# Kernel optimization log

Hardware: AMD Instinct MI355X
Metric: run time of the kernel (lower is better)

## Reference

```python
import jax, jax.numpy as jnp
import numpy as np

B, D, E = 2048, 2048, 64
EPS = 1e-8

def setup_inputs() -> dict:
    key = jax.random.key(0)
    kx, kw, kb = jax.random.split(key, 3)
    # scale weights like torch Linear default init (uniform ~ 1/sqrt(D)); use scaled normal
    return {
        "x": jax.random.normal(kx, (B, D), dtype=jnp.float32),
        "W": jax.random.normal(kw, (E * E, D), dtype=jnp.float32) / np.sqrt(D),
        "b": jax.random.normal(kb, (E * E,), dtype=jnp.float32) / np.sqrt(D),
        "reg": jnp.asarray(0.01, dtype=jnp.float32),
    }

def reference(x, W, b, reg):
    # Linear projection: [B, D] @ [D, E*E] + b -> [B, E*E]
    m = jnp.einsum("bd,ed->be", x, W) + b
    m = m.reshape(-1, E, E)
    # Symmetrize and regularize diagonal
    m = (m + jnp.swapaxes(m, 1, 2)) * 0.5
    m = m + reg * jnp.eye(E, dtype=m.dtype)
    # Batched symmetric eigendecomposition (ascending eigenvalues)
    eigenvals = jnp.linalg.eigvalsh(m)  # [B, E]
    # Descending order, log-clamped
    eigenvals = jnp.flip(eigenvals, axis=1)
    return jnp.log(jnp.clip(eigenvals, EPS, None))
```

## Files before the change

### kernel.cpp

```cpp
#include <hip/hip_runtime.h>

typedef __bf16 bf16x8 __attribute__((ext_vector_type(8)));
typedef float f32x4 __attribute__((ext_vector_type(4)));

union U8 { uint4 u; bf16x8 b; };

__device__ inline float bf16f(unsigned short h) {
    return __uint_as_float(((unsigned)h) << 16);
}

__device__ inline unsigned short f32_to_bf16_rn(float f) {
    unsigned u = __float_as_uint(f);
    unsigned rounding = 0x7FFFu + ((u >> 16) & 1u);
    u += rounding;
    return (unsigned short)(u >> 16);
}

__device__ inline double wsum(double v) {
    #pragma unroll
    for (int m = 32; m; m >>= 1) v += __shfl_xor(v, m, 64);
    return v;
}
__device__ inline double wmin(double v) {
    #pragma unroll
    for (int m = 32; m; m >>= 1) v = fmin(v, __shfl_xor(v, m, 64));
    return v;
}
__device__ inline double wmax(double v) {
    #pragma unroll
    for (int m = 32; m; m >>= 1) v = fmax(v, __shfl_xor(v, m, 64));
    return v;
}

#define AS1C(p) ((const __attribute__((address_space(1))) void*)(p))
#define AS3(p)  ((__attribute__((address_space(3))) void*)(p))

__global__ __launch_bounds__(256) void split2(
    const float* __restrict__ X, const float* __restrict__ W,
    const float* __restrict__ b, const float* __restrict__ regp,
    unsigned short* __restrict__ Xh, unsigned short* __restrict__ Xm, unsigned short* __restrict__ Xl,
    unsigned short* __restrict__ Sh, unsigned short* __restrict__ Sm, unsigned short* __restrict__ Sl,
    float* __restrict__ bsym)
{
    size_t i4 = (size_t)blockIdx.x * 256 + threadIdx.x;

    if (i4 < 1048576) {
        float4 v = ((const float4*)X)[i4];
        ushort4 h, m, l; float r1;
        h.x = f32_to_bf16_rn(v.x); r1 = v.x - bf16f(h.x);
        m.x = f32_to_bf16_rn(r1);  l.x = f32_to_bf16_rn(r1 - bf16f(m.x));
        h.y = f32_to_bf16_rn(v.y); r1 = v.y - bf16f(h.y);
        m.y = f32_to_bf16_rn(r1);  l.y = f32_to_bf16_rn(r1 - bf16f(m.y));
        h.z = f32_to_bf16_rn(v.z); r1 = v.z - bf16f(h.z);
        m.z = f32_to_bf16_rn(r1);  l.z = f32_to_bf16_rn(r1 - bf16f(m.z));
        h.w = f32_to_bf16_rn(v.w); r1 = v.w - bf16f(h.w);
        m.w = f32_to_bf16_rn(r1);  l.w = f32_to_bf16_rn(r1 - bf16f(m.w));
        ((ushort4*)Xh)[i4] = h;
        ((ushort4*)Xm)[i4] = m;
        ((ushort4*)Xl)[i4] = l;
        return;
    }

    size_t q = i4 - 1048576;
    int p  = (int)(q >> 9);
    int d4 = (int)(q & 511);

    if (p >= 2080) {
        ushort4 z; z.x = 0; z.y = 0; z.z = 0; z.w = 0;
        ((ushort4*)Sh)[q] = z; ((ushort4*)Sm)[q] = z; ((ushort4*)Sl)[q] = z;
        if (d4 == 0) bsym[p] = 0.0f;
        return;
    }

    double sd = sqrt(16641.0 - 8.0 * (double)p);
    int i = (int)((129.0 - sd) * 0.5);
    if (i < 0) i = 0;
    if (i > 63) i = 63;
    while (i < 63 && ((i + 1) * (128 - i)) / 2 <= p) ++i;
    while (i > 0 && (i * (129 - i)) / 2 > p) --i;
    int j = i + (p - (i * (129 - i)) / 2);
    int e1 = i * 64 + j;
    int e2 = j * 64 + i;

    float4 v1 = ((const float4*)W)[(size_t)e1 * 512 + d4];
    float4 v2 = ((const float4*)W)[(size_t)e2 * 512 + d4];
    float4 v;
    v.x = 0.5f * (v1.x + v2.x);
    v.y = 0.5f * (v1.y + v2.y);
    v.z = 0.5f * (v1.z + v2.z);
    v.w = 0.5f * (v1.w + v2.w);

    ushort4 h, m, l; float r1;
    h.x = f32_to_bf16_rn(v.x); r1 = v.x - bf16f(h.x);
    m.x = f32_to_bf16_rn(r1);  l.x = f32_to_bf16_rn(r1 - bf16f(m.x));
    h.y = f32_to_bf16_rn(v.y); r1 = v.y - bf16f(h.y);
    m.y = f32_to_bf16_rn(r1);  l.y = f32_to_bf16_rn(r1 - bf16f(m.y));
    h.z = f32_to_bf16_rn(v.z); r1 = v.z - bf16f(h.z);
    m.z = f32_to_bf16_rn(r1);  l.z = f32_to_bf16_rn(r1 - bf16f(m.z));
    h.w = f32_to_bf16_rn(v.w); r1 = v.w - bf16f(h.w);
    m.w = f32_to_bf16_rn(r1);  l.w = f32_to_bf16_rn(r1 - bf16f(m.w));
    ((ushort4*)Sh)[q] = h;
    ((ushort4*)Sm)[q] = m;
    ((ushort4*)Sl)[q] = l;

    if (d4 == 0)
        bsym[p] = 0.5f * (b[e1] + b[e2]) + ((i == j) ? regp[0] : 0.0f);
}

__global__ __launch_bounds__(256) void gemm_packed(
    const unsigned short* __restrict__ Xh, const unsigned short* __restrict__ Xm,
    const unsigned short* __restrict__ Xl,
    const unsigned short* __restrict__ Sh, const unsigned short* __restrict__ Sm,
    const unsigned short* __restrict__ Sl,
    const float* __restrict__ bsym, float* __restrict__ Mp)
{
    const int K = 2048, NP = 2112;
    __shared__ unsigned short S[18432];

    int tid  = threadIdx.x;
    int id   = blockIdx.x;
    int c    = id & 7;
    int sid  = id >> 3;
    int wg   = c * 66 + sid;
    int bx   = wg % 33;
    int by   = wg / 33;
    int m0   = by * 128;
    int n0   = bx * 64;

    int wave = tid >> 6;
    int lane = tid & 63;
    int l16  = lane & 15;
    int quad = lane >> 4;
    int wm   = wave * 32;

    const unsigned short* gpA[3];
    const unsigned short* gpB[3];
    gpA[0] = Xh + (size_t)m0 * K;
    gpA[1] = Xm + (size_t)m0 * K;
    gpA[2] = Xl + (size_t)m0 * K;
    gpB[0] = Sh + (size_t)n0 * K;
    gpB[1] = Sm + (size_t)n0 * K;
    gpB[2] = Sl + (size_t)n0 * K;

    int rA = lane >> 2;
    int cA = (lane & 3) << 3;

    f32x4 acc[2][4];
    #pragma unroll
    for (int mi = 0; mi < 2; ++mi)
        #pragma unroll
        for (int ni = 0; ni < 4; ++ni)
            acc[mi][ni] = f32x4{0.f, 0.f, 0.f, 0.f};

    for (int k0 = 0; k0 < K; k0 += 32) {
        __syncthreads();
        #pragma unroll
        for (int p = 0; p < 3; ++p) {
            #pragma unroll
            for (int q = 0; q < 2; ++q) {
                const unsigned short* g = gpA[p] + (size_t)(32 * wave + 16 * q + rA) * K + k0 + cA;
                char* l = (char*)S + p * 8192 + wave * 2048 + q * 1024;
                __builtin_amdgcn_global_load_lds(AS1C(g), AS3(l), 16, 0, 0);
            }
            {
                const unsigned short* g = gpB[p] + (size_t)(16 * wave + rA) * K + k0 + cA;
                char* l = (char*)S + 24576 + p * 4096 + wave * 1024;
                __builtin_amdgcn_global_load_lds(AS1C(g), AS3(l), 16, 0, 0);
            }
        }
        __syncthreads();

        U8 ah[2], am[2], al[2], bh[4], bm[4], bl[4];
        #pragma unroll
        for (int mi = 0; mi < 2; ++mi) {
            int ro = (wm + mi * 16 + l16) * 32 + quad * 8;
            ah[mi].u = *(const uint4*)&S[ro];
            am[mi].u = *(const uint4*)&S[4096 + ro];
            al[mi].u = *(const uint4*)&S[8192 + ro];
        }
        #pragma unroll
        for (int ni = 0; ni < 4; ++ni) {
            int ro = (ni * 16 + l16) * 32 + quad * 8;
            bh[ni].u = *(const uint4*)&S[12288 + ro];
            bm[ni].u = *(const uint4*)&S[14336 + ro];
            bl[ni].u = *(const uint4*)&S[16384 + ro];
        }

        #pragma unroll
        for (int mi = 0; mi < 2; ++mi)
            #pragma unroll
            for (int ni = 0; ni < 4; ++ni) {
                acc[mi][ni] = __builtin_amdgcn_mfma_f32_16x16x32_bf16(
                    al[mi].b, bh[ni].b, acc[mi][ni], 0, 0, 0);
                acc[mi][ni] = __builtin_amdgcn_mfma_f32_16x16x32_bf16(
                    ah[mi].b, bl[ni].b, acc[mi][ni], 0, 0, 0);
                acc[mi][ni] = __builtin_amdgcn_mfma_f32_16x16x32_bf16(
                    am[mi].b, bm[ni].b, acc[mi][ni], 0, 0, 0);
                acc[mi][ni] = __builtin_amdgcn_mfma_f32_16x16x32_bf16(
                    am[mi].b, bh[ni].b, acc[mi][ni], 0, 0, 0);
                acc[mi][ni] = __builtin_amdgcn_mfma_f32_16x16x32_bf16(
                    ah[mi].b, bm[ni].b, acc[mi][ni], 0, 0, 0);
                acc[mi][ni] = __builtin_amdgcn_mfma_f32_16x16x32_bf16(
                    ah[mi].b, bh[ni].b, acc[mi][ni], 0, 0, 0);
            }
    }

    #pragma unroll
    for (int ni = 0; ni < 4; ++ni) {
        int col = n0 + ni * 16 + l16;
        float bv = bsym[col];
        #pragma unroll
        for (int mi = 0; mi < 2; ++mi) {
            int row = m0 + wm + mi * 16 + quad * 4;
            #pragma unroll
            for (int r = 0; r < 4; ++r)
                Mp[(size_t)(row + r) * NP + col] = acc[mi][ni][r] + bv;
        }
    }
}

__global__ __launch_bounds__(128, 4) void tridiag_packed2(
    const float* __restrict__ Mp, double* __restrict__ trid)
{
    __shared__ __align__(16) float Ls[2112];
    __shared__ __align__(16) double rowb[64];
    __shared__ __align__(16) double ubuf[64];
    __shared__ __align__(16) double wbuf[64];
    __shared__ __align__(16) double pps[128];
    __shared__ double dbuf[64];
    __shared__ double ebuf[64];

    int g   = blockIdx.x;
    int tid = threadIdx.x;
    int h   = tid >> 6;
    int t   = tid & 63;
    int base = 32 * h;

    const float4* Pg = (const float4*)(Mp + (size_t)g * 2112);
    float4* L4 = (float4*)Ls;
    #pragma unroll
    for (int s = 0; s < 4; ++s)
        L4[s * 128 + tid] = Pg[s * 128 + tid];
    if (tid < 16) L4[512 + tid] = Pg[512 + tid];
    __syncthreads();

    double A[32];
    #pragma unroll
    for (int jj = 0; jj < 32; ++jj) {
        int cj = base + jj;
        int lo = (t < cj) ? t : cj;
        int hi = t + cj - lo;
        int idx = ((lo * (129 - lo)) >> 1) + (hi - lo);
        A[jj] = (double)Ls[idx];
    }

    #pragma unroll 1
    for (int k = 0; k < 32; ++k) {
        if (t == k) {
            #pragma unroll
            for (int jj = 0; jj < 16; ++jj)
                *(double2*)&rowb[base + 2 * jj] = double2{A[2 * jj], A[2 * jj + 1]};
        }
        __syncthreads();

        double x  = rowb[t];
        double x1 = rowb[k + 1];
        double xm = (t > k) ? x : 0.0;
        double sigma = wsum(xm * xm);

        double alpha = 0.0, u = 0.0, w = 0.0, rK = 0.0;
        bool run = (sigma > 1e-300);
        if (run) {
            double sq = sqrt(sigma);
            alpha = (x1 >= 0.0) ? -sq : sq;
            rK = 1.0 / (sigma - x1 * alpha);
            u = (t == k + 1) ? (x - alpha) : xm;
        }
        if (h == 0) ubuf[t] = u;
        if (tid == 0) { dbuf[k] = rowb[k]; ebuf[k] = alpha; }
        __syncthreads();

        double ph = 0.0;
        if (run) {
            double p0 = 0.0, p1 = 0.0;
            #pragma unroll
            for (int jj = 0; jj < 16; ++jj) {
                double2 uv = *(const double2*)&ubuf[base + 2 * jj];
                p0 += A[2 * jj]     * uv.x;
                p1 += A[2 * jj + 1] * uv.y;
            }
            ph = p0 + p1;
        }
        pps[h * 64 + t] = ph;
        __syncthreads();

        if (run) {
            double p = (t > k) ? (pps[t] + pps[64 + t]) * rK : 0.0;
            double cc = wsum(u * p) * (0.5 * rK);
            w = p - cc * u;
        }
        if (h == 0) wbuf[t] = w;
        __syncthreads();

        if (run) {
            #pragma unroll
            for (int jj = 0; jj < 16; ++jj) {
                double2 uv = *(const double2*)&ubuf[base + 2 * jj];
                double2 wv = *(const double2*)&wbuf[base + 2 * jj];
                A[2 * jj]     -= u * wv.x + w * uv.x;
                A[2 * jj + 1] -= u * wv.y + w * uv.y;
            }
        }
    }

    #pragma unroll 1
    for (int k = 32; k < 62; ++k) {
        if (h == 1 && t == k) {
            #pragma unroll
            for (int jj = 0; jj < 16; ++jj)
                *(double2*)&rowb[32 + 2 * jj] = double2{A[2 * jj], A[2 * jj + 1]};
        }
        __syncthreads();

        double u = 0.0, w = 0.0, rK = 0.0;
        bool run = false;
        if (h == 1) {
            double x  = rowb[t];
            double x1 = rowb[k + 1];
            double xm = (t > k) ? x : 0.0;
            double sigma = wsum(xm * xm);
            double alpha = 0.0;
            run = (sigma > 1e-300);
            if (run) {
                double sq = sqrt(sigma);
                alpha = (x1 >= 0.0) ? -sq : sq;
                rK = 1.0 / (sigma - x1 * alpha);
                u = (t == k + 1) ? (x - alpha) : xm;
            }
            ubuf[t] = u;
            if (t == 0) { dbuf[k] = rowb[k]; ebuf[k] = alpha; }
        }
        __syncthreads();

        if (h == 1) {
            if (run) {
                double p0 = 0.0, p1 = 0.0;
                #pragma unroll
                for (int jj = 0; jj < 16; ++jj) {
                    double2 uv = *(const double2*)&ubuf[32 + 2 * jj];
                    p0 += A[2 * jj]     * uv.x;
                    p1 += A[2 * jj + 1] * uv.y;
                }
                double p = (t > k) ? (p0 + p1) * rK : 0.0;
                double cc = wsum(u * p) * (0.5 * rK);
                w = p - cc * u;
            }
            wbuf[t] = w;
        }
        __syncthreads();

        if (h == 1 && run) {
            #pragma unroll
            for (int jj = 0; jj < 16; ++jj) {
                double2 uv = *(const double2*)&ubuf[32 + 2 * jj];
                double2 wv = *(const double2*)&wbuf[32 + 2 * jj];
                A[2 * jj]     -= u * wv.x + w * uv.x;
                A[2 * jj + 1] -= u * wv.y + w * uv.y;
            }
        }
    }

    if (h == 1 && t == 62) dbuf[62] = A[30];
    if (h == 1 && t == 63) { dbuf[63] = A[31];
                             ebuf[62] = A[30]; }
    if (tid == 0) ebuf[63] = 0.0;
    __syncthreads();

    if (h == 0) {
        double* tg = trid + (size_t)g * 128;
        tg[t]      = dbuf[t];
        tg[64 + t] = ebuf[t];
    }
}

__global__ __launch_bounds__(256) void gemm_bt(const float* __restrict__ Xf,
                                               const float* __restrict__ Wf,
                                               const float* __restrict__ biasf,
                                               float* __restrict__ M)
{
    const int K = 2048, N = 4096;
    __shared__ unsigned short AsH[128][32];
    __shared__ unsigned short AsM[128][32];
    __shared__ unsigned short AsL[128][32];
    __shared__ unsigned short BsH[128][32];
    __shared__ unsigned short BsM[128][32];
    __shared__ unsigned short BsL[128][32];

    int tid  = threadIdx.x;
    int m0   = blockIdx.y * 128;
    int n0   = blockIdx.x * 128;
    int wid  = tid >> 6;
    int lane = tid & 63;
    int wm   = (wid >> 1) * 64;
    int wn   = (wid & 1) * 64;
    int l16  = lane & 15;
    int quad = lane >> 4;

    f32x4 acc[4][4];
    #pragma unroll
    for (int mi = 0; mi < 4; ++mi)
        #pragma unroll
        for (int ni = 0; ni < 4; ++ni)
            acc[mi][ni] = f32x4{0.f, 0.f, 0.f, 0.f};

    for (int k0 = 0; k0 < K; k0 += 32) {
        #pragma unroll
        for (int s = 0; s < 4; ++s) {
            int c  = tid + s * 256;
            int r  = c >> 3;
            int kc = (c & 7) << 2;
            {
                float4 v = *(const float4*)&Xf[(size_t)(m0 + r) * K + k0 + kc];
                ushort4 h, mm_, l; float r1;
                h.x = f32_to_bf16_rn(v.x); r1 = v.x - bf16f(h.x);
                mm_.x = f32_to_bf16_rn(r1); l.x = f32_to_bf16_rn(r1 - bf16f(mm_.x));
                h.y = f32_to_bf16_rn(v.y); r1 = v.y - bf16f(h.y);
                mm_.y = f32_to_bf16_rn(r1); l.y = f32_to_bf16_rn(r1 - bf16f(mm_.y));
                h.z = f32_to_bf16_rn(v.z); r1 = v.z - bf16f(h.z);
                mm_.z = f32_to_bf16_rn(r1); l.z = f32_to_bf16_rn(r1 - bf16f(mm_.z));
                h.w = f32_to_bf16_rn(v.w); r1 = v.w - bf16f(h.w);
                mm_.w = f32_to_bf16_rn(r1); l.w = f32_to_bf16_rn(r1 - bf16f(mm_.w));
                *(ushort4*)&AsH[r][kc] = h; *(ushort4*)&AsM[r][kc] = mm_; *(ushort4*)&AsL[r][kc] = l;
            }
            {
                float4 v = *(const float4*)&Wf[(size_t)(n0 + r) * K + k0 + kc];
                ushort4 h, mm_, l; float r1;
                h.x = f32_to_bf16_rn(v.x); r1 = v.x - bf16f(h.x);
                mm_.x = f32_to_bf16_rn(r1); l.x = f32_to_bf16_rn(r1 - bf16f(mm_.x));
                h.y = f32_to_bf16_rn(v.y); r1 = v.y - bf16f(h.y);
                mm_.y = f32_to_bf16_rn(r1); l.y = f32_to_bf16_rn(r1 - bf16f(mm_.y));
                h.z = f32_to_bf16_rn(v.z); r1 = v.z - bf16f(h.z);
                mm_.z = f32_to_bf16_rn(r1); l.z = f32_to_bf16_rn(r1 - bf16f(mm_.z));
                h.w = f32_to_bf16_rn(v.w); r1 = v.w - bf16f(h.w);
                mm_.w = f32_to_bf16_rn(r1); l.w = f32_to_bf16_rn(r1 - bf16f(mm_.w));
                *(ushort4*)&BsH[r][kc] = h; *(ushort4*)&BsM[r][kc] = mm_; *(ushort4*)&BsL[r][kc] = l;
            }
        }
        __syncthreads();

        U8 ah[4], am[4], al[4], bh[4], bm[4], bl[4];
        #pragma unroll
        for (int mi = 0; mi < 4; ++mi) {
            ah[mi].u = *(const uint4*)&AsH[wm + mi * 16 + l16][quad * 8];
            am[mi].u = *(const uint4*)&AsM[wm + mi * 16 + l16][quad * 8];
            al[mi].u = *(const uint4*)&AsL[wm + mi * 16 + l16][quad * 8];
        }
        #pragma unroll
        for (int ni = 0; ni < 4; ++ni) {
            bh[ni].u = *(const uint4*)&BsH[wn + ni * 16 + l16][quad * 8];
            bm[ni].u = *(const uint4*)&BsM[wn + ni * 16 + l16][quad * 8];
            bl[ni].u = *(const uint4*)&BsL[wn + ni * 16 + l16][quad * 8];
        }

        #pragma unroll
        for (int mi = 0; mi < 4; ++mi)
            #pragma unroll
            for (int ni = 0; ni < 4; ++ni) {
                acc[mi][ni] = __builtin_amdgcn_mfma_f32_16x16x32_bf16(al[mi].b, bh[ni].b, acc[mi][ni], 0, 0, 0);
                acc[mi][ni] = __builtin_amdgcn_mfma_f32_16x16x32_bf16(ah[mi].b, bl[ni].b, acc[mi][ni], 0, 0, 0);
                acc[mi][ni] = __builtin_amdgcn_mfma_f32_16x16x32_bf16(am[mi].b, bm[ni].b, acc[mi][ni], 0, 0, 0);
                acc[mi][ni] = __builtin_amdgcn_mfma_f32_16x16x32_bf16(am[mi].b, bh[ni].b, acc[mi][ni], 0, 0, 0);
                acc[mi][ni] = __builtin_amdgcn_mfma_f32_16x16x32_bf16(ah[mi].b, bm[ni].b, acc[mi][ni], 0, 0, 0);
                acc[mi][ni] = __builtin_amdgcn_mfma_f32_16x16x32_bf16(ah[mi].b, bh[ni].b, acc[mi][ni], 0, 0, 0);
            }
        __syncthreads();
    }

    #pragma unroll
    for (int ni = 0; ni < 4; ++ni) {
        int col = n0 + wn + ni * 16 + l16;
        float bv = biasf[col];
        #pragma unroll
        for (int mi = 0; mi < 4; ++mi) {
            int row = m0 + wm + mi * 16 + quad * 4;
            #pragma unroll
            for (int r = 0; r < 4; ++r)
                M[(size_t)(row + r) * N + col] = acc[mi][ni][r] + bv;
        }
    }
}

__global__ __launch_bounds__(64, 2) void tridiag_full(const float* __restrict__ M,
                                                      const float* __restrict__ regf,
                                                      double* __restrict__ trid)
{
    __shared__ float Ms[64][65];
    __shared__ __align__(16) double rowb[64];
    __shared__ __align__(16) double ubuf[64];
    __shared__ __align__(16) double wbuf[64];
    __shared__ double dbuf[64];
    __shared__ double ebuf[64];

    int g = blockIdx.x;
    int t = threadIdx.x;
    const float* Mg = M + (size_t)g * 4096;

    for (int r = 0; r < 64; ++r)
        Ms[r][t] = Mg[r * 64 + t];
    __syncthreads();

    double regv = (double)regf[0];
    double A[64];
    #pragma unroll
    for (int j = 0; j < 64; ++j)
        A[j] = 0.5 * ((double)Ms[t][j] + (double)Ms[j][t]);
    #pragma unroll
    for (int j = 0; j < 64; ++j)
        A[j] += (j == t) ? regv : 0.0;

    #pragma unroll 1
    for (int k = 0; k < 62; ++k) {
        if (t == k) {
            #pragma unroll
            for (int j = 0; j < 32; ++j)
                *(double2*)&rowb[2 * j] = double2{A[2 * j], A[2 * j + 1]};
        }
        __syncthreads();

        double s0 = 0.0, s1 = 0.0;
        #pragma unroll
        for (int j = 0; j < 64; ++j) {
            double aj = (j > k) ? A[j] : 0.0;
            if (j & 1) s1 += aj * aj; else s0 += aj * aj;
        }
        double sigma = __shfl(s0 + s1, k, 64);
        double x  = rowb[t];
        double x1 = __shfl(x, k + 1, 64);

        double alpha = 0.0, u = 0.0, w = 0.0, Kh = 1.0;
        bool run = (sigma > 1e-300);
        if (run) {
            double sq = sqrt(sigma);
            alpha = (x1 >= 0.0) ? -sq : sq;
            Kh = sigma - x1 * alpha;
            u = (t == k + 1) ? (x - alpha) : ((t > k) ? x : 0.0);
        }
        ubuf[t] = u;
        if (t == 0) { dbuf[k] = rowb[k]; ebuf[k] = alpha; }
        __syncthreads();

        if (run) {
            double p0 = 0.0, p1 = 0.0;
            #pragma unroll
            for (int j = 0; j < 32; ++j) {
                double2 uv = *(const double2*)&ubuf[2 * j];
                p0 += A[2 * j]     * uv.x;
                p1 += A[2 * j + 1] * uv.y;
            }
            double p = (t > k) ? (p0 + p1) / Kh : 0.0;
            double cc = wsum(u * p) / (2.0 * Kh);
            w = p - cc * u;
        }
        wbuf[t] = w;
        __syncthreads();

        if (run) {
            #pragma unroll
            for (int j = 0; j < 32; ++j) {
                double2 uv = *(const double2*)&ubuf[2 * j];
                double2 wv = *(const double2*)&wbuf[2 * j];
                A[2 * j]     -= u * wv.x + w * uv.x;
                A[2 * j + 1] -= u * wv.y + w * uv.y;
            }
        }
        __syncthreads();
    }

    if (t == 62) dbuf[62] = A[62];
    if (t == 63) { dbuf[63] = A[63]; ebuf[62] = A[62]; }
    if (t == 0)  ebuf[63] = 0.0;
    __syncthreads();

    double* tg = trid + (size_t)g * 128;
    tg[t]      = dbuf[t];
    tg[64 + t] = ebuf[t];
}

__global__ __launch_bounds__(64) void bisect_kernel(const double* __restrict__ trid,
                                                    float* __restrict__ out)
{
    __shared__ double dd[64];
    __shared__ double e2[64];
    __shared__ double ea[64];

    int g = blockIdx.x;
    int t = threadIdx.x;
    const double* tg = trid + (size_t)g * 128;

    double dv = tg[t];
    double ev = tg[64 + t];
    dd[t] = dv;
    ea[t] = fabs(ev);
    e2[t] = ev * ev;
    __syncthreads();

    double el  = (t > 0) ? ea[t - 1] : 0.0;
    double er  = (t < 63) ? ea[t] : 0.0;
    double rad = el + er;
    double lo = wmin(dv - rad);
    double hi = wmax(dv + rad);
    double mid0 = 0.5 * (lo + hi);
    double half = (0.5 * (hi - lo) + 1e-12) * 1.0000001;
    double a = mid0 - half;
    double b = mid0 + half;

    for (int it = 0; it < 30; ++it) {
        double xm = 0.5 * (a + b);
        double pm = 1.0;
        double p  = dd[0] - xm;
        int cnt = (p < 0.0);
        #pragma unroll
        for (int i = 1; i < 64; ++i) {
            double pi = (dd[i] - xm) * p - e2[i - 1] * pm;
            cnt += ((pi < 0.0) != (p < 0.0));
            double ap = fabs(pi);
            double s = (ap > 1e150) ? 1e-150 : ((ap < 1e-150) ? 1e150 : 1.0);
            pm = p * s;
            p  = pi * s;
        }
        if (cnt > t) b = xm; else a = xm;
    }

    double lam = 0.5 * (a + b);
    double v = fmax(lam, 1e-8);
    out[(size_t)g * 64 + (63 - t)] = (float)log(v);
}

extern "C" void kernel_launch(void* const* d_in, const int* in_sizes, int n_in,
                              void* d_out, int out_size, void* d_ws, size_t ws_size,
                              hipStream_t stream)
{
    const float* X    = (const float*)d_in[0];
    const float* Wt   = (const float*)d_in[1];
    const float* bias = (const float*)d_in[2];
    const float* regp = (const float*)d_in[3];

    char* w = (char*)d_ws;
    float* out = (float*)d_out;

    const size_t NEED_FAST = 70525184ull;
    if (ws_size >= NEED_FAST) {
        float*  Mp   = (float*)w;
        double* trid = (double*)(w + 17301504);
        unsigned short* Xh = (unsigned short*)(w + 19398656);
        unsigned short* Xm = (unsigned short*)(w + 27787264);
        unsigned short* Xl = (unsigned short*)(w + 36175872);
        unsigned short* Sh = (unsigned short*)(w + 44564480);
        unsigned short* Sm = (unsigned short*)(w + 53215232);
        unsigned short* Sl = (unsigned short*)(w + 61865984);
        float* bsym = (float*)(w + 70516736);
        split2<<<dim3(8320), dim3(256), 0, stream>>>(X, Wt, bias, regp,
                                                     Xh, Xm, Xl, Sh, Sm, Sl, bsym);
        gemm_packed<<<dim3(528), dim3(256), 0, stream>>>(Xh, Xm, Xl, Sh, Sm, Sl, bsym, Mp);
        tridiag_packed2<<<dim3(2048), dim3(128), 0, stream>>>(Mp, trid);
        bisect_kernel<<<dim3(2048), dim3(64), 0, stream>>>(trid, out);
    } else {
        float*  M    = (float*)w;
        double* trid = (double*)(w + 33554432);
        gemm_bt<<<dim3(32, 16), dim3(256), 0, stream>>>(X, Wt, bias, M);
        tridiag_full<<<dim3(2048), dim3(64), 0, stream>>>(M, regp, trid);
        bisect_kernel<<<dim3(2048), dim3(64), 0, stream>>>(trid, out);
    }
}
```

Before: 609.4 us.

## Split GEMM along K into two partial outputs and streamline tridiagonalization reductions

After: 651.6 us. 6.9% more time.

```diff
diff --git a/kernel.cpp b/kernel.cpp
--- a/kernel.cpp
+++ b/kernel.cpp
@@ -30,6 +30,36 @@
     #pragma unroll
     for (int m = 32; m; m >>= 1) v = fmax(v, __shfl_xor(v, m, 64));
     return v;
+}
+
+__device__ inline double dpp_sum64(double v) {
+    union DU { double d; int i[2]; };
+    DU x, t; x.d = v;
+    t.i[0] = __builtin_amdgcn_update_dpp(0, x.i[0], 0xB1, 0xF, 0xF, true);
+    t.i[1] = __builtin_amdgcn_update_dpp(0, x.i[1], 0xB1, 0xF, 0xF, true);
+    x.d += t.d;
+    t.i[0] = __builtin_amdgcn_update_dpp(0, x.i[0], 0x4E, 0xF, 0xF, true);
+    t.i[1] = __builtin_amdgcn_update_dpp(0, x.i[1], 0x4E, 0xF, 0xF, true);
+    x.d += t.d;
+    t.i[0] = __builtin_amdgcn_update_dpp(0, x.i[0], 0x141, 0xF, 0xF, true);
+    t.i[1] = __builtin_amdgcn_update_dpp(0, x.i[1], 0x141, 0xF, 0xF, true);
+    x.d += t.d;
+    t.i[0] = __builtin_amdgcn_update_dpp(0, x.i[0], 0x140, 0xF, 0xF, true);
+    t.i[1] = __builtin_amdgcn_update_dpp(0, x.i[1], 0x140, 0xF, 0xF, true);
+    x.d += t.d;
+    t.i[0] = __builtin_amdgcn_update_dpp(0, x.i[0], 0x142, 0xF, 0xF, true);
+    t.i[1] = __builtin_amdgcn_update_dpp(0, x.i[1], 0x142, 0xF, 0xF, true);
+    x.d += t.d;
+    t.i[0] = __builtin_amdgcn_update_dpp(0, x.i[0], 0x143, 0xF, 0xF, true);
+    t.i[1] = __builtin_amdgcn_update_dpp(0, x.i[1], 0x143, 0xF, 0xF, true);
+    x.d += t.d;
+    int lo = __builtin_amdgcn_readlane(x.i[0], 63);
+    int hi = __builtin_amdgcn_readlane(x.i[1], 63);
+    return __hiloint2double(hi, lo);
+}
+
+__device__ inline float4 f4add(float4 a, float4 b) {
+    return float4{a.x + b.x, a.y + b.y, a.z + b.z, a.w + b.w};
 }
 
 #define AS1C(p) ((const __attribute__((address_space(1))) void*)(p))
@@ -121,11 +151,14 @@
     int id   = blockIdx.x;
     int c    = id & 7;
     int sid  = id >> 3;
-    int wg   = c * 66 + sid;
+    int kh   = (sid >= 66) ? 1 : 0;
+    int sidh = sid - kh * 66;
+    int wg   = c * 66 + sidh;
     int bx   = wg % 33;
     int by   = wg / 33;
     int m0   = by * 128;
     int n0   = bx * 64;
+    int kb   = kh * 1024;
 
     int wave = tid >> 6;
     int lane = tid & 63;
@@ -152,7 +185,7 @@
         for (int ni = 0; ni < 4; ++ni)
             acc[mi][ni] = f32x4{0.f, 0.f, 0.f, 0.f};
 
-    for (int k0 = 0; k0 < K; k0 += 32) {
+    for (int k0 = kb; k0 < kb + 1024; k0 += 32) {
         __syncthreads();
         #pragma unroll
         for (int p = 0; p < 3; ++p) {
@@ -205,28 +238,28 @@
             }
     }
 
+    float* Mout = Mp + (size_t)kh * 4325376;
     #pragma unroll
     for (int ni = 0; ni < 4; ++ni) {
         int col = n0 + ni * 16 + l16;
-        float bv = bsym[col];
+        float bv = kh ? 0.0f : bsym[col];
         #pragma unroll
         for (int mi = 0; mi < 2; ++mi) {
             int row = m0 + wm + mi * 16 + quad * 4;
             #pragma unroll
             for (int r = 0; r < 4; ++r)
-                Mp[(size_t)(row + r) * NP + col] = acc[mi][ni][r] + bv;
-        }
-    }
-}
-
-__global__ __launch_bounds__(128, 4) void tridiag_packed2(
+                Mout[(size_t)(row + r) * NP + col] = acc[mi][ni][r] + bv;
+        }
+    }
+}
+
+__global__ __launch_bounds__(128, 3) void tridiag_packed3(
     const float* __restrict__ Mp, double* __restrict__ trid)
 {
     __shared__ __align__(16) float Ls[2112];
     __shared__ __align__(16) double rowb[64];
-    __shared__ __align__(16) double ubuf[64];
     __shared__ __align__(16) double wbuf[64];
-    __shared__ __align__(16) double pps[128];
+    __shared__ __align__(16) double pps2[128];
     __shared__ double dbuf[64];
     __shared__ double ebuf[64];
 
@@ -236,12 +269,13 @@
     int t   = tid & 63;
     int base = 32 * h;
 
-    const float4* Pg = (const float4*)(Mp + (size_t)g * 2112);
+    const float4* Pg0 = (const float4*)(Mp + (size_t)g * 2112);
+    const float4* Pg1 = (const float4*)(Mp + 4325376 + (size_t)g * 2112);
     float4* L4 = (float4*)Ls;
     #pragma unroll
     for (int s = 0; s < 4; ++s)
-        L4[s * 128 + tid] = Pg[s * 128 + tid];
-    if (tid < 16) L4[512 + tid] = Pg[512 + tid];
+        L4[s * 128 + tid] = f4add(Pg0[s * 128 + tid], Pg1[s * 128 + tid]);
+    if (tid < 16) L4[512 + tid] = f4add(Pg0[512 + tid], Pg1[512 + tid]);
     __syncthreads();
 
     double A[32];
@@ -266,49 +300,50 @@
         double x  = rowb[t];
         double x1 = rowb[k + 1];
         double xm = (t > k) ? x : 0.0;
-        double sigma = wsum(xm * xm);
-
+        double sigma = dpp_sum64(xm * xm);
+
+        bool run = (sigma > 1e-300);
         double alpha = 0.0, u = 0.0, w = 0.0, rK = 0.0;
-        bool run = (sigma > 1e-300);
+        double uc[32];
+        double ph = 0.0;
         if (run) {
             double sq = sqrt(sigma);
             alpha = (x1 >= 0.0) ? -sq : sq;
             rK = 1.0 / (sigma - x1 * alpha);
             u = (t == k + 1) ? (x - alpha) : xm;
-        }
-        if (h == 0) ubuf[t] = u;
+            double p0 = 0.0, p1 = 0.0;
+            #pragma unroll
+            for (int jj = 0; jj < 16; ++jj) {
+                double2 rv = *(const double2*)&rowb[base + 2 * jj];
+                int j0 = base + 2 * jj, j1 = base + 2 * jj + 1;
+                double u0 = (j0 == k + 1) ? (rv.x - alpha) : ((j0 > k) ? rv.x : 0.0);
+                double u1 = (j1 == k + 1) ? (rv.y - alpha) : ((j1 > k) ? rv.y : 0.0);
+                uc[2 * jj]     = u0;
+                uc[2 * jj + 1] = u1;
+                p0 += A[2 * jj]     * u0;
+                p1 += A[2 * jj + 1] * u1;
+            }
+            ph = p0 + p1;
+        }
+        pps2[2 * t + h] = ph;
         if (tid == 0) { dbuf[k] = rowb[k]; ebuf[k] = alpha; }
         __syncthreads();
 
-        double ph = 0.0;
         if (run) {
-            double p0 = 0.0, p1 = 0.0;
+            double2 pp = *(const double2*)&pps2[2 * t];
+            double p = (t > k) ? (pp.x + pp.y) * rK : 0.0;
+            double cc = dpp_sum64(u * p) * (0.5 * rK);
+            w = p - cc * u;
+        }
+        if (h == 0) wbuf[t] = w;
+        __syncthreads();
+
+        if (run) {
             #pragma unroll
             for (int jj = 0; jj < 16; ++jj) {
-                double2 uv = *(const double2*)&ubuf[base + 2 * jj];
-                p0 += A[2 * jj]     * uv.x;
-                p1 += A[2 * jj + 1] * uv.y;
-            }
-            ph = p0 + p1;
-        }
-        pps[h * 64 + t] = ph;
-        __syncthreads();
-
-        if (run) {
-            double p = (t > k) ? (pps[t] + pps[64 + t]) * rK : 0.0;
-            double cc = wsum(u * p) * (0.5 * rK);
-            w = p - cc * u;
-        }
-        if (h == 0) wbuf[t] = w;
-        __syncthreads();
-
-        if (run) {
-            #pragma unroll
-            for (int jj = 0; jj < 16; ++jj) {
-                double2 uv = *(const double2*)&ubuf[base + 2 * jj];
                 double2 wv = *(const double2*)&wbuf[base + 2 * jj];
-                A[2 * jj]     -= u * wv.x + w * uv.x;
-                A[2 * jj + 1] -= u * wv.y + w * uv.y;
+                A[2 * jj]     -= u * wv.x + w * uc[2 * jj];
+                A[2 * jj + 1] -= u * wv.y + w * uc[2 * jj + 1];
             }
         }
     }
@@ -322,50 +357,48 @@
         }
         __syncthreads();
 
-        double u = 0.0, w = 0.0, rK = 0.0;
+        double u = 0.0, w = 0.0;
         bool run = false;
+        double uc[32];
         if (h == 1) {
             double x  = rowb[t];
             double x1 = rowb[k + 1];
             double xm = (t > k) ? x : 0.0;
-            double sigma = wsum(xm * xm);
+            double sigma = dpp_sum64(xm * xm);
             double alpha = 0.0;
             run = (sigma > 1e-300);
             if (run) {
                 double sq = sqrt(sigma);
                 alpha = (x1 >= 0.0) ? -sq : sq;
-                rK = 1.0 / (sigma - x1 * alpha);
+                double rK = 1.0 / (sigma - x1 * alpha);
                 u = (t == k + 1) ? (x - alpha) : xm;
-            }
-            ubuf[t] = u;
-            if (t == 0) { dbuf[k] = rowb[k]; ebuf[k] = alpha; }
-        }
-        __syncthreads();
-
-        if (h == 1) {
-            if (run) {
                 double p0 = 0.0, p1 = 0.0;
                 #pragma unroll
                 for (int jj = 0; jj < 16; ++jj) {
-                    double2 uv = *(const double2*)&ubuf[32 + 2 * jj];
-                    p0 += A[2 * jj]     * uv.x;
-                    p1 += A[2 * jj + 1] * uv.y;
+                    double2 rv = *(const double2*)&rowb[32 + 2 * jj];
+                    int j0 = 32 + 2 * jj, j1 = 33 + 2 * jj;
+                    double u0 = (j0 == k + 1) ? (rv.x - alpha) : ((j0 > k) ? rv.x : 0.0);
+                    double u1 = (j1 == k + 1) ? (rv.y - alpha) : ((j1 > k) ? rv.y : 0.0);
+                    uc[2 * jj]     = u0;
+                    uc[2 * jj + 1] = u1;
+                    p0 += A[2 * jj]     * u0;
+                    p1 += A[2 * jj + 1] * u1;
                 }
                 double p = (t > k) ? (p0 + p1) * rK : 0.0;
-                double cc = wsum(u * p) * (0.5 * rK);
+                double cc = dpp_sum64(u * p) * (0.5 * rK);
                 w = p - cc * u;
             }
             wbuf[t] = w;
+            if (t == 0) { dbuf[k] = rowb[k]; ebuf[k] = alpha; }
         }
         __syncthreads();
 
         if (h == 1 && run) {
             #pragma unroll
             for (int jj = 0; jj < 16; ++jj) {
-                double2 uv = *(const double2*)&ubuf[32 + 2 * jj];
                 double2 wv = *(const double2*)&wbuf[32 + 2 * jj];
-                A[2 * jj]     -= u * wv.x + w * uv.x;
-                A[2 * jj + 1] -= u * wv.y + w * uv.y;
+                A[2 * jj]     -= u * wv.x + w * uc[2 * jj];
+                A[2 * jj + 1] -= u * wv.y + w * uc[2 * jj + 1];
             }
         }
     }
@@ -648,21 +681,21 @@
     char* w = (char*)d_ws;
     float* out = (float*)d_out;
 
-    const size_t NEED_FAST = 70525184ull;
+    const size_t NEED_FAST = 87826688ull;
     if (ws_size >= NEED_FAST) {
         float*  Mp   = (float*)w;
-        double* trid = (double*)(w + 17301504);
-        unsigned short* Xh = (unsigned short*)(w + 19398656);
-        unsigned short* Xm = (unsigned short*)(w + 27787264);
-        unsigned short* Xl = (unsigned short*)(w + 36175872);
-        unsigned short* Sh = (unsigned short*)(w + 44564480);
-        unsigned short* Sm = (unsigned short*)(w + 53215232);
-        unsigned short* Sl = (unsigned short*)(w + 61865984);
-        float* bsym = (float*)(w + 70516736);
+        double* trid = (double*)(w + 34603008);
+        unsigned short* Xh = (unsigned short*)(w + 36700160);
+        unsigned short* Xm = (unsigned short*)(w + 45088768);
+        unsigned short* Xl = (unsigned short*)(w + 53477376);
+        unsigned short* Sh = (unsigned short*)(w + 61865984);
+        unsigned short* Sm = (unsigned short*)(w + 70516736);
+        unsigned short* Sl = (unsigned short*)(w + 79167488);
+        float* bsym = (float*)(w + 87818240);
         split2<<<dim3(8320), dim3(256), 0, stream>>>(X, Wt, bias, regp,
                                                      Xh, Xm, Xl, Sh, Sm, Sl, bsym);
-        gemm_packed<<<dim3(528), dim3(256), 0, stream>>>(Xh, Xm, Xl, Sh, Sm, Sl, bsym, Mp);
-        tridiag_packed2<<<dim3(2048), dim3(128), 0, stream>>>(Mp, trid);
+        gemm_packed<<<dim3(1056), dim3(256), 0, stream>>>(Xh, Xm, Xl, Sh, Sm, Sl, bsym, Mp);
+        tridiag_packed3<<<dim3(2048), dim3(128), 0, stream>>>(Mp, trid);
         bisect_kernel<<<dim3(2048), dim3(64), 0, stream>>>(trid, out);
     } else {
         float*  M    = (float*)w;
```
